# Kernel tuning notes

Measured on AMD Instinct MI355X. Metric: run time of the kernel, lower is better.

The kernel has to match this reference:

```python
import jax, jax.numpy as jnp
import numpy as np

RAD = 0.15          # sphere radius (init kwarg)
MIN_DIST = 2.0 * RAD  # two spheres collide when center distance < 2*rad


def setup_inputs() -> dict:
    key = jax.random.key(0)
    pos = jax.random.normal(key, (64, 1024, 3), dtype=jnp.float32)  # [T, N, 3]
    return {"pos": pos}


def reference(pos):
    """Sphere collision check equivalent to the sweep-and-prune CUDA kernel.

    The CUDA kernel sorts along one axis purely as an acceleration structure;
    the math it computes is: over all unordered robot pairs (i<j) at each
    timestep, a pair collides if ||p_i - p_j|| < 2*rad. Returns
      count: total number of colliding pairs (int)
      loss:  sum over colliding pairs of (2*rad - dist)^2 penetration penalty
    """
    T, N, _ = pos.shape
    diff = pos[:, :, None, :] - pos[:, None, :, :]          # [T, N, N, 3]
    dist2 = jnp.sum(diff * diff, axis=-1)                   # [T, N, N]
    iu = jnp.triu(jnp.ones((N, N), dtype=bool), k=1)        # i < j, exclude self
    colliding = iu[None, :, :] & (dist2 < MIN_DIST * MIN_DIST)
    # safe sqrt (diagonal / coincident points have dist2 == 0)
    safe_d2 = jnp.where(dist2 > 0.0, dist2, 1.0)
    dist = jnp.sqrt(safe_d2)
    pen = MIN_DIST - dist                                   # penetration depth
    loss = jnp.sum(jnp.where(colliding, pen * pen, 0.0))
    count = jnp.sum(colliding).astype(jnp.int32)
    return (count, loss)
```

## Files before the change

kernel.cpp:

```cpp
#include <hip/hip_runtime.h>
#include <math.h>

#define TN     64
#define NP     1024
#define RADIUS 0.15f
#define MIN_D  (2.0f * RADIUS)
#define R2     (MIN_D * MIN_D)

#define SPLIT  16
#define GI     16
#define NGRP   (NP / GI)
#define GPB    (NGRP / SPLIT)
#define BLOCK  256
#define NBLK   (TN * SPLIT)

#define FLAG_MAGIC 0x5EED5EEDu

__launch_bounds__(BLOCK, 4)
__global__ void fused_kernel(const float* __restrict__ pos,
                             unsigned int* __restrict__ ws,
                             float* __restrict__ out) {
    __shared__ float sh[NP * 3];
    const int bid   = blockIdx.x;
    const int t     = bid / SPLIT;
    const int split = bid % SPLIT;
    const int tid   = threadIdx.x;

    const float4* p4  = (const float4*)(pos + (size_t)t * NP * 3);
    float4*       sh4 = (float4*)sh;
    #pragma unroll
    for (int i = 0; i < (NP * 3 / 4) / BLOCK; ++i)
        sh4[tid + i * BLOCK] = p4[tid + i * BLOCK];
    __syncthreads();

    unsigned int cnt = 0;
    float loss = 0.0f;

    #pragma unroll
    for (int m = 0; m < GPB; ++m) {
        const int g = (m & 1) ? (m * SPLIT + (SPLIT - 1 - split))
                              : (m * SPLIT + split);
        const int b = g * GI;

        float xi[GI], yi[GI], zi[GI];
        #pragma unroll
        for (int k = 0; k < GI; ++k) {
            xi[k] = sh[3 * (b + k) + 0];
            yi[k] = sh[3 * (b + k) + 1];
            zi[k] = sh[3 * (b + k) + 2];
        }
        #pragma unroll
        for (int k = 0; k < GI; ++k)
            asm volatile("" : "+v"(xi[k]), "+v"(yi[k]), "+v"(zi[k]));

        if (tid < GI - 1) {
            const int j = b + 1 + tid;
            const float xj = sh[3 * j], yj = sh[3 * j + 1], zj = sh[3 * j + 2];
            #pragma unroll
            for (int k = 0; k < GI; ++k) {
                if (k <= tid) {
                    const float dx = xi[k] - xj;
                    const float dy = yi[k] - yj;
                    const float dz = zi[k] - zj;
                    const float d2 = dx * dx + dy * dy + dz * dz;
                    cnt += (d2 < R2) ? 1u : 0u;
                    const float pen = fmaxf(MIN_D - __builtin_amdgcn_sqrtf(d2), 0.0f);
                    loss += pen * pen;
                }
            }
        }

        #pragma unroll 2
        for (int j = b + GI + tid; j < NP; j += BLOCK) {
            const float xj = sh[3 * j], yj = sh[3 * j + 1], zj = sh[3 * j + 2];
            #pragma unroll
            for (int k = 0; k < GI; ++k) {
                const float dx = xi[k] - xj;
                const float dy = yi[k] - yj;
                const float dz = zi[k] - zj;
                const float d2 = dx * dx + dy * dy + dz * dz;
                cnt += (d2 < R2) ? 1u : 0u;
                const float pen = fmaxf(MIN_D - __builtin_amdgcn_sqrtf(d2), 0.0f);
                loss += pen * pen;
            }
        }
    }

    float fcnt = (float)cnt;
    #pragma unroll
    for (int off = 32; off > 0; off >>= 1) {
        fcnt += __shfl_down(fcnt, off);
        loss += __shfl_down(loss, off);
    }
    __shared__ float cs[BLOCK / 64], ls[BLOCK / 64];
    const int wave = tid >> 6;
    if ((tid & 63) == 0) { cs[wave] = fcnt; ls[wave] = loss; }
    __syncthreads();

    if (tid == 0) {
        float c = 0.0f, l = 0.0f;
        #pragma unroll
        for (int w = 0; w < BLOCK / 64; ++w) { c += cs[w]; l += ls[w]; }
        __hip_atomic_store(&ws[3 * bid + 0], __float_as_uint(c),
                           __ATOMIC_RELAXED, __HIP_MEMORY_SCOPE_AGENT);
        __hip_atomic_store(&ws[3 * bid + 1], __float_as_uint(l),
                           __ATOMIC_RELAXED, __HIP_MEMORY_SCOPE_AGENT);
        __hip_atomic_store(&ws[3 * bid + 2], FLAG_MAGIC,
                           __ATOMIC_RELEASE, __HIP_MEMORY_SCOPE_AGENT);
    }

    if (bid != 0) return;

    __syncthreads();
    float sc = 0.0f, sl = 0.0f;
    #pragma unroll
    for (int i = 0; i < NBLK / BLOCK; ++i) {
        const int s = tid + i * BLOCK;
        while (__hip_atomic_load(&ws[3 * s + 2], __ATOMIC_ACQUIRE,
                                 __HIP_MEMORY_SCOPE_AGENT) != FLAG_MAGIC) { }
        sc += __uint_as_float(__hip_atomic_load(&ws[3 * s + 0], __ATOMIC_RELAXED,
                                                __HIP_MEMORY_SCOPE_AGENT));
        sl += __uint_as_float(__hip_atomic_load(&ws[3 * s + 1], __ATOMIC_RELAXED,
                                                __HIP_MEMORY_SCOPE_AGENT));
    }
    #pragma unroll
    for (int off = 32; off > 0; off >>= 1) {
        sc += __shfl_down(sc, off);
        sl += __shfl_down(sl, off);
    }
    if ((tid & 63) == 0) { cs[wave] = sc; ls[wave] = sl; }
    __syncthreads();
    if (tid == 0) {
        float ct = 0.0f, lt = 0.0f;
        #pragma unroll
        for (int w = 0; w < BLOCK / 64; ++w) { ct += cs[w]; lt += ls[w]; }
        out[0] = ct;
        out[1] = lt;
    }
}

extern "C" void kernel_launch(void* const* d_in, const int* in_sizes, int n_in,
                              void* d_out, int out_size, void* d_ws, size_t ws_size,
                              hipStream_t stream) {
    const float*  pos = (const float*)d_in[0];
    unsigned int* ws  = (unsigned int*)d_ws;
    float*        out = (float*)d_out;

    fused_kernel<<<NBLK, BLOCK, 0, stream>>>(pos, ws, out);
}
```

Baseline: 74.62 us.

## Pad shared positions to float4 and load group points as scalar uniforms

```diff
diff --git a/kernel.cpp b/kernel.cpp
--- a/kernel.cpp
+++ b/kernel.cpp
@@ -20,48 +20,54 @@
 __global__ void fused_kernel(const float* __restrict__ pos,
                              unsigned int* __restrict__ ws,
                              float* __restrict__ out) {
-    __shared__ float sh[NP * 3];
+    __shared__ float4 shp[NP];
     const int bid   = blockIdx.x;
     const int t     = bid / SPLIT;
     const int split = bid % SPLIT;
     const int tid   = threadIdx.x;
 
-    const float4* p4  = (const float4*)(pos + (size_t)t * NP * 3);
-    float4*       sh4 = (float4*)sh;
-    #pragma unroll
-    for (int i = 0; i < (NP * 3 / 4) / BLOCK; ++i)
-        sh4[tid + i * BLOCK] = p4[tid + i * BLOCK];
+    {
+        const float4* p4 = (const float4*)(pos + (size_t)t * NP * 3);
+        const float4 a = p4[3 * tid + 0];
+        const float4 b = p4[3 * tid + 1];
+        const float4 c = p4[3 * tid + 2];
+        shp[4 * tid + 0] = make_float4(a.x, a.y, a.z, 0.0f);
+        shp[4 * tid + 1] = make_float4(a.w, b.x, b.y, 0.0f);
+        shp[4 * tid + 2] = make_float4(b.z, b.w, c.x, 0.0f);
+        shp[4 * tid + 3] = make_float4(c.y, c.z, c.w, 0.0f);
+    }
     __syncthreads();
 
     unsigned int cnt = 0;
     float loss = 0.0f;
 
-    #pragma unroll
+    #pragma unroll 1
     for (int m = 0; m < GPB; ++m) {
         const int g = (m & 1) ? (m * SPLIT + (SPLIT - 1 - split))
                               : (m * SPLIT + split);
         const int b = g * GI;
 
+        const float* tp = pos + (size_t)t * NP * 3 + 3 * b;
         float xi[GI], yi[GI], zi[GI];
         #pragma unroll
         for (int k = 0; k < GI; ++k) {
-            xi[k] = sh[3 * (b + k) + 0];
-            yi[k] = sh[3 * (b + k) + 1];
-            zi[k] = sh[3 * (b + k) + 2];
+            xi[k] = tp[3 * k + 0];
+            yi[k] = tp[3 * k + 1];
+            zi[k] = tp[3 * k + 2];
         }
         #pragma unroll
         for (int k = 0; k < GI; ++k)
-            asm volatile("" : "+v"(xi[k]), "+v"(yi[k]), "+v"(zi[k]));
+            asm volatile("" : "+s"(xi[k]), "+s"(yi[k]), "+s"(zi[k]));
 
         if (tid < GI - 1) {
             const int j = b + 1 + tid;
-            const float xj = sh[3 * j], yj = sh[3 * j + 1], zj = sh[3 * j + 2];
+            const float4 pj = shp[j];
             #pragma unroll
             for (int k = 0; k < GI; ++k) {
                 if (k <= tid) {
-                    const float dx = xi[k] - xj;
-                    const float dy = yi[k] - yj;
-                    const float dz = zi[k] - zj;
+                    const float dx = xi[k] - pj.x;
+                    const float dy = yi[k] - pj.y;
+                    const float dz = zi[k] - pj.z;
                     const float d2 = dx * dx + dy * dy + dz * dz;
                     cnt += (d2 < R2) ? 1u : 0u;
                     const float pen = fmaxf(MIN_D - __builtin_amdgcn_sqrtf(d2), 0.0f);
@@ -72,12 +78,12 @@
 
         #pragma unroll 2
         for (int j = b + GI + tid; j < NP; j += BLOCK) {
-            const float xj = sh[3 * j], yj = sh[3 * j + 1], zj = sh[3 * j + 2];
+            const float4 pj = shp[j];
             #pragma unroll
             for (int k = 0; k < GI; ++k) {
-                const float dx = xi[k] - xj;
-                const float dy = yi[k] - yj;
-                const float dz = zi[k] - zj;
+                const float dx = xi[k] - pj.x;
+                const float dy = yi[k] - pj.y;
+                const float dz = zi[k] - pj.z;
                 const float d2 = dx * dx + dy * dy + dz * dz;
                 cnt += (d2 < R2) ? 1u : 0u;
                 const float pen = fmaxf(MIN_D - __builtin_amdgcn_sqrtf(d2), 0.0f);
```

Result: no change. 74.39 us (-0.3%).
